# Kernel tuning notes

Hardware: AMD Instinct MI355X
Metric: run time of the kernel (lower is better)

## Reference

```python
import jax, jax.numpy as jnp
import numpy as np

N_TX, N_ACC, E = 500000, 100000, 1000000
D_TX, D_ACC, H = 64, 32, 64


def setup_inputs() -> dict:
    key = jax.random.key(0)
    ks = jax.random.split(key, 16)
    s = 0.05
    return {
        "x_tx": jax.random.normal(ks[0], (N_TX, D_TX), jnp.float32),
        "x_acc": jax.random.normal(ks[1], (N_ACC, D_ACC), jnp.float32),
        "pays_src": jax.random.randint(ks[2], (E,), 0, N_ACC),
        "pays_dst": jax.random.randint(ks[3], (E,), 0, N_TX),
        "rev_src": jax.random.randint(ks[4], (E,), 0, N_TX),
        "rev_dst": jax.random.randint(ks[5], (E,), 0, N_ACC),
        # SAGEConv for ('account','pays','transaction'): lin_l: D_ACC->H (bias), lin_r: D_TX->H (no bias)
        "Wl_pays": jax.random.normal(ks[6], (D_ACC, H), jnp.float32) * s,
        "bl_pays": jnp.zeros((H,), jnp.float32),
        "Wr_pays": jax.random.normal(ks[7], (D_TX, H), jnp.float32) * s,
        # SAGEConv for ('transaction','rev_pays','account'): lin_l: D_TX->H, lin_r: D_ACC->H
        "Wl_rev": jax.random.normal(ks[8], (D_TX, H), jnp.float32) * s,
        "bl_rev": jnp.zeros((H,), jnp.float32),
        "Wr_rev": jax.random.normal(ks[9], (D_ACC, H), jnp.float32) * s,
        # output head Linear(H, 1)
        "W_out": jax.random.normal(ks[10], (H, 1), jnp.float32) * s,
        "b_out": jnp.zeros((1,), jnp.float32),
    }


def _segment_mean(msg, dst, n_dst):
    # scatter-mean: sum per dst node / clamped degree (isolated nodes -> 0)
    s = jax.ops.segment_sum(msg, dst, num_segments=n_dst)
    c = jax.ops.segment_sum(jnp.ones((dst.shape[0], 1), msg.dtype), dst, num_segments=n_dst)
    return s / jnp.maximum(c, 1.0)


def _sage(x_src, x_dst, src, dst, Wl, bl, Wr):
    agg = _segment_mean(x_src[src], dst, x_dst.shape[0])  # [n_dst, d_src]
    return agg @ Wl + bl + x_dst @ Wr  # [n_dst, H]


def reference(x_tx, x_acc, pays_src, pays_dst, rev_src, rev_dst,
              Wl_pays, bl_pays, Wr_pays, Wl_rev, bl_rev, Wr_rev, W_out, b_out):
    # HeteroConv: each dst node type receives exactly one edge type here, so aggr='mean' is identity
    h_tx = _sage(x_acc, x_tx, pays_src, pays_dst, Wl_pays, bl_pays, Wr_pays)
    h_acc = _sage(x_tx, x_acc, rev_src, rev_dst, Wl_rev, bl_rev, Wr_rev)
    tx_x = jax.nn.relu(h_tx)
    _ = jax.nn.relu(h_acc)  # computed by the module but unused downstream
    logits = (tx_x @ W_out + b_out)[:, 0]
    return logits, tx_x
```

## Files before the change

kernel.cpp:

```cpp
#include <hip/hip_runtime.h>

#define N_TX   500000
#define N_ACC  100000
#define E_CNT  1000000
#define D_TX   64
#define D_ACC  32
#define H_DIM  64

#define SCAN_B    256
#define SCAN_I    8
#define SCAN_TILE (SCAN_B * SCAN_I)
#define NSCAN_BLOCKS ((N_TX + SCAN_TILE - 1) / SCAN_TILE)


__global__ __launch_bounds__(256) void hist_kernel(
    const int* __restrict__ dst, int* __restrict__ cnt) {
    int e = blockIdx.x * blockDim.x + threadIdx.x;
    if (e < E_CNT) atomicAdd(&cnt[dst[e]], 1);
}

__global__ __launch_bounds__(SCAN_B) void scan1_kernel(
    const int* __restrict__ cnt, int* __restrict__ offs, int* __restrict__ bsum) {
    __shared__ int lds[SCAN_B];
    int base = blockIdx.x * SCAN_TILE + threadIdx.x * SCAN_I;
    int v[SCAN_I];
    int tsum = 0;
#pragma unroll
    for (int i = 0; i < SCAN_I; ++i) {
        int idx = base + i;
        v[i] = (idx < N_TX) ? cnt[idx] : 0;
        tsum += v[i];
    }
    lds[threadIdx.x] = tsum;
    __syncthreads();
    for (int off = 1; off < SCAN_B; off <<= 1) {
        int a = 0;
        if ((int)threadIdx.x >= off) a = lds[threadIdx.x - off];
        __syncthreads();
        lds[threadIdx.x] += a;
        __syncthreads();
    }
    int texcl = lds[threadIdx.x] - tsum;
    if (threadIdx.x == SCAN_B - 1) bsum[blockIdx.x] = lds[SCAN_B - 1];
    int run = texcl;
#pragma unroll
    for (int i = 0; i < SCAN_I; ++i) {
        int idx = base + i;
        if (idx < N_TX) offs[idx] = run;
        run += v[i];
    }
}

__global__ __launch_bounds__(256) void scan2_kernel(int* __restrict__ bsum, int nb) {
    __shared__ int lds[256];
    int t = threadIdx.x;
    int v = (t < nb) ? bsum[t] : 0;
    lds[t] = v;
    __syncthreads();
    for (int off = 1; off < 256; off <<= 1) {
        int a = 0;
        if (t >= off) a = lds[t - off];
        __syncthreads();
        lds[t] += a;
        __syncthreads();
    }
    if (t < nb) bsum[t] = lds[t] - v;
}

__global__ __launch_bounds__(256) void finalize_kernel(
    int* __restrict__ offs, int* __restrict__ cursors, const int* __restrict__ bsum) {
    int i = blockIdx.x * blockDim.x + threadIdx.x;
    if (i < N_TX) {
        int f = offs[i] + bsum[i / SCAN_TILE];
        offs[i] = f;
        cursors[i] = f;
    }
}

__global__ __launch_bounds__(256) void fill_kernel(
    const int* __restrict__ src, const int* __restrict__ dst,
    int* __restrict__ cursors, int* __restrict__ eidx) {
    int e = blockIdx.x * blockDim.x + threadIdx.x;
    if (e < E_CNT) {
        int d = dst[e];
        int p = atomicAdd(&cursors[d], 1);
        eidx[p] = src[e];
    }
}

__global__ __launch_bounds__(256, 4) void acc_transform_kernel(
    const float* __restrict__ x_acc, const float* __restrict__ Wl,
    float* __restrict__ y, int rows_per_wave) {
    int lane = threadIdx.x & 63;
    int wave = (blockIdx.x * blockDim.x + threadIdx.x) >> 6;
    float wl[D_ACC];
#pragma unroll
    for (int k = 0; k < D_ACC; ++k) wl[k] = Wl[k * H_DIM + lane];
#pragma unroll
    for (int k = 0; k < D_ACC; ++k) asm volatile("" : "+v"(wl[k]));
    int r0 = wave * rows_per_wave;
    int r1 = min(r0 + rows_per_wave, N_ACC);
    for (int row = r0; row < r1; ++row) {
        int urow = __builtin_amdgcn_readfirstlane(row);
        const float4* xr = (const float4*)(x_acc + (size_t)urow * D_ACC);
        float a0 = 0.f, a1 = 0.f, a2 = 0.f, a3 = 0.f;
#pragma unroll
        for (int q = 0; q < 8; ++q) {
            float4 v = xr[q];
            a0 = fmaf(v.x, wl[4 * q + 0], a0);
            a1 = fmaf(v.y, wl[4 * q + 1], a1);
            a2 = fmaf(v.z, wl[4 * q + 2], a2);
            a3 = fmaf(v.w, wl[4 * q + 3], a3);
        }
        y[(size_t)urow * H_DIM + lane] = (a0 + a1) + (a2 + a3);
    }
}

__global__ __launch_bounds__(256, 4) void row_kernel(
    const float* __restrict__ x_tx,
    const float* __restrict__ y,
    const int*   __restrict__ offs,
    const int*   __restrict__ cnt,
    const int*   __restrict__ eidx,
    const float* __restrict__ Wr,
    const float* __restrict__ bl,
    const float* __restrict__ Wout,
    const float* __restrict__ bout,
    float*       __restrict__ logits,
    float*       __restrict__ txx,
    int rows_per_wave) {
    int lane = threadIdx.x & 63;
    int wave = (blockIdx.x * blockDim.x + threadIdx.x) >> 6;

    float wr[D_TX];
#pragma unroll
    for (int k = 0; k < D_TX; ++k) wr[k] = Wr[k * H_DIM + lane];
#pragma unroll
    for (int k = 0; k < D_TX; ++k) asm volatile("" : "+v"(wr[k]));
    float b  = bl[lane];
    float wo = Wout[lane];
    float bo = bout[0];
    asm volatile("" : "+v"(b), "+v"(wo), "+v"(bo));

    int r0 = wave * rows_per_wave;
    int r1 = min(r0 + rows_per_wave, N_TX);
    for (int row = r0; row < r1; ++row) {
        int urow = __builtin_amdgcn_readfirstlane(row);
        int deg = __builtin_amdgcn_readfirstlane(cnt[urow]);
        int off = __builtin_amdgcn_readfirstlane(offs[urow]);

        float g = 0.f, v = 0.f;
        if (deg > 0) {
            int s0 = __builtin_amdgcn_readfirstlane(eidx[off]);
            v = y[(size_t)s0 * H_DIM + lane];
        }

        const float4* xr = (const float4*)(x_tx + (size_t)urow * D_TX);
        float a0 = 0.f, a1 = 0.f, a2 = 0.f, a3 = 0.f;
#pragma unroll
        for (int q = 0; q < 16; ++q) {
            float4 xv = xr[q];
            a0 = fmaf(xv.x, wr[4 * q + 0], a0);
            a1 = fmaf(xv.y, wr[4 * q + 1], a1);
            a2 = fmaf(xv.z, wr[4 * q + 2], a2);
            a3 = fmaf(xv.w, wr[4 * q + 3], a3);
        }

        for (int e = 1; e < deg; ++e) {
            int s2 = __builtin_amdgcn_readfirstlane(eidx[off + e]);
            float v2 = y[(size_t)s2 * H_DIM + lane];
            g += v;
            v = v2;
        }
        if (deg > 0) g += v;

        float inv = 1.0f / (float)(deg > 0 ? deg : 1);
        float h = ((a0 + a1) + (a2 + a3)) + b + g * inv;
        float r = fmaxf(h, 0.f);
        txx[(size_t)urow * H_DIM + lane] = r;

        float p = r * wo;
#pragma unroll
        for (int sh = 32; sh > 0; sh >>= 1) p += __shfl_down(p, sh);
        if (lane == 0) logits[urow] = p + bo;
    }
}

extern "C" void kernel_launch(void* const* d_in, const int* in_sizes, int n_in,
                              void* d_out, int out_size, void* d_ws, size_t ws_size,
                              hipStream_t stream) {
    const float* x_tx     = (const float*)d_in[0];
    const float* x_acc    = (const float*)d_in[1];
    const int*   pays_src = (const int*)d_in[2];
    const int*   pays_dst = (const int*)d_in[3];
    const float* Wl   = (const float*)d_in[6];
    const float* bl   = (const float*)d_in[7];
    const float* Wr   = (const float*)d_in[8];
    const float* Wout = (const float*)d_in[12];
    const float* bout = (const float*)d_in[13];

    float* out    = (float*)d_out;
    float* logits = out;
    float* txx    = out + N_TX;

    int* cnt     = (int*)d_ws;
    int* offs    = cnt + N_TX;
    int* cursors = offs + N_TX;
    int* bsum    = cursors + N_TX;
    int* eidx    = bsum + 1024;
    float* y     = (float*)(eidx + E_CNT);

    hipMemsetAsync(cnt, 0, (size_t)N_TX * sizeof(int), stream);

    hist_kernel<<<(E_CNT + 255) / 256, 256, 0, stream>>>(pays_dst, cnt);
    scan1_kernel<<<NSCAN_BLOCKS, SCAN_B, 0, stream>>>(cnt, offs, bsum);
    scan2_kernel<<<1, 256, 0, stream>>>(bsum, NSCAN_BLOCKS);
    finalize_kernel<<<(N_TX + 255) / 256, 256, 0, stream>>>(offs, cursors, bsum);
    fill_kernel<<<(E_CNT + 255) / 256, 256, 0, stream>>>(pays_src, pays_dst, cursors, eidx);

    {
        const int blocks = 1024;
        int rpw = (N_ACC + blocks * 4 - 1) / (blocks * 4);
        acc_transform_kernel<<<blocks, 256, 0, stream>>>(x_acc, Wl, y, rpw);
    }

    {
        const int blocks = 2048;
        int rpw = (N_TX + blocks * 4 - 1) / (blocks * 4);
        row_kernel<<<blocks, 256, 0, stream>>>(
            x_tx, y, offs, cnt, eidx, Wr, bl, Wout, bout, logits, txx, rpw);
    }
}
```

Baseline: 667.7 us.

## Batch-prefetch per-row CSR metadata and first four neighbor indices across lanes

Each wave in row_kernel now owns exactly 64 rows. It loads degree, offset and up to the first four neighbor indices for all 64 rows in one vectorised per-lane load. Inside the loop it pulls them out with readlane, and the up-to-four neighbor gathers are issued together, replacing the serial scalar-load-dependent chain. This cuts load latency per row, at the cost of more registers and a different grid size. The acc_transform grid is also doubled.

```diff
diff --git a/kernel.cpp b/kernel.cpp
--- a/kernel.cpp
+++ b/kernel.cpp
@@ -127,10 +127,13 @@
     const float* __restrict__ Wout,
     const float* __restrict__ bout,
     float*       __restrict__ logits,
-    float*       __restrict__ txx,
-    int rows_per_wave) {
+    float*       __restrict__ txx) {
     int lane = threadIdx.x & 63;
     int wave = (blockIdx.x * blockDim.x + threadIdx.x) >> 6;
+
+    int rbase = wave * 64;
+    if (rbase >= N_TX) return;
+    int nrows = min(64, N_TX - rbase);
 
     float wr[D_TX];
 #pragma unroll
@@ -142,18 +145,33 @@
     float bo = bout[0];
     asm volatile("" : "+v"(b), "+v"(wo), "+v"(bo));
 
-    int r0 = wave * rows_per_wave;
-    int r1 = min(r0 + rows_per_wave, N_TX);
-    for (int row = r0; row < r1; ++row) {
-        int urow = __builtin_amdgcn_readfirstlane(row);
-        int deg = __builtin_amdgcn_readfirstlane(cnt[urow]);
-        int off = __builtin_amdgcn_readfirstlane(offs[urow]);
-
-        float g = 0.f, v = 0.f;
-        if (deg > 0) {
-            int s0 = __builtin_amdgcn_readfirstlane(eidx[off]);
-            v = y[(size_t)s0 * H_DIM + lane];
-        }
+    int deg_l = 0, off_l = 0;
+    if (lane < nrows) {
+        deg_l = cnt[rbase + lane];
+        off_l = offs[rbase + lane];
+    }
+    int s0_l = 0, s1_l = 0, s2_l = 0, s3_l = 0;
+    if (deg_l > 0) s0_l = eidx[off_l];
+    if (deg_l > 1) s1_l = eidx[off_l + 1];
+    if (deg_l > 2) s2_l = eidx[off_l + 2];
+    if (deg_l > 3) s3_l = eidx[off_l + 3];
+
+    int ubase = __builtin_amdgcn_readfirstlane(rbase);
+
+    for (int k = 0; k < nrows; ++k) {
+        int urow = ubase + k;
+        int deg = __builtin_amdgcn_readlane(deg_l, k);
+        int off = __builtin_amdgcn_readlane(off_l, k);
+        int s0  = __builtin_amdgcn_readlane(s0_l, k);
+        int s1  = __builtin_amdgcn_readlane(s1_l, k);
+        int s2  = __builtin_amdgcn_readlane(s2_l, k);
+        int s3  = __builtin_amdgcn_readlane(s3_l, k);
+
+        float v0 = 0.f, v1 = 0.f, v2 = 0.f, v3 = 0.f;
+        if (deg > 0) v0 = y[(size_t)s0 * H_DIM + lane];
+        if (deg > 1) v1 = y[(size_t)s1 * H_DIM + lane];
+        if (deg > 2) v2 = y[(size_t)s2 * H_DIM + lane];
+        if (deg > 3) v3 = y[(size_t)s3 * H_DIM + lane];
 
         const float4* xr = (const float4*)(x_tx + (size_t)urow * D_TX);
         float a0 = 0.f, a1 = 0.f, a2 = 0.f, a3 = 0.f;
@@ -166,13 +184,11 @@
             a3 = fmaf(xv.w, wr[4 * q + 3], a3);
         }
 
-        for (int e = 1; e < deg; ++e) {
-            int s2 = __builtin_amdgcn_readfirstlane(eidx[off + e]);
-            float v2 = y[(size_t)s2 * H_DIM + lane];
-            g += v;
-            v = v2;
+        float g = (v0 + v1) + (v2 + v3);
+        for (int e = 4; e < deg; ++e) {
+            int se = __builtin_amdgcn_readfirstlane(eidx[off + e]);
+            g += y[(size_t)se * H_DIM + lane];
         }
-        if (deg > 0) g += v;
 
         float inv = 1.0f / (float)(deg > 0 ? deg : 1);
         float h = ((a0 + a1) + (a2 + a3)) + b + g * inv;
@@ -219,15 +235,15 @@
     fill_kernel<<<(E_CNT + 255) / 256, 256, 0, stream>>>(pays_src, pays_dst, cursors, eidx);
 
     {
-        const int blocks = 1024;
+        const int blocks = 2048;
         int rpw = (N_ACC + blocks * 4 - 1) / (blocks * 4);
         acc_transform_kernel<<<blocks, 256, 0, stream>>>(x_acc, Wl, y, rpw);
     }
 
     {
-        const int blocks = 2048;
-        int rpw = (N_TX + blocks * 4 - 1) / (blocks * 4);
+        const int waves  = (N_TX + 63) / 64;
+        const int blocks = (waves + 3) / 4;
         row_kernel<<<blocks, 256, 0, stream>>>(
-            x_tx, y, offs, cnt, eidx, Wr, bl, Wout, bout, logits, txx, rpw);
-    }
-}
+            x_tx, y, offs, cnt, eidx, Wr, bl, Wout, bout, logits, txx);
+    }
+}
```

Result: faster. 628.2 us (-5.9%).
